# Optimization experiments

Measured on AMD Instinct MI355X. Metric: run time of the kernel, lower is better.

Reference implementation:

```python
import jax, jax.numpy as jnp
import numpy as np

H = 1024

def setup_inputs() -> dict:
    key = jax.random.key(0)
    ks = jax.random.split(key, 7)
    B, S = 64, 2048
    decoder_hidden = jax.random.normal(ks[0], (B, H), dtype=jnp.float32)
    encoder_outputs = jax.random.normal(ks[1], (B, S, H), dtype=jnp.float32)
    sc = 1.0 / np.sqrt(H)
    W1_w = jax.random.normal(ks[2], (H, H), dtype=jnp.float32) * sc
    W1_b = jax.random.normal(ks[3], (H,), dtype=jnp.float32) * sc
    W2_w = jax.random.normal(ks[4], (H, H), dtype=jnp.float32) * sc
    W2_b = jax.random.normal(ks[5], (H,), dtype=jnp.float32) * sc
    v_w = jax.random.normal(ks[6], (H,), dtype=jnp.float32) * sc
    return {"decoder_hidden": decoder_hidden, "encoder_outputs": encoder_outputs,
            "W1_w": W1_w, "W1_b": W1_b, "W2_w": W2_w, "W2_b": W2_b, "v_w": v_w}

def reference(decoder_hidden, encoder_outputs, W1_w, W1_b, W2_w, W2_b, v_w):
    # enc proj: [B,S,H] @ [H,H] ; dec proj: [B,H] @ [H,H], broadcast over S
    enc_proj = jnp.einsum('bsh,hk->bsk', encoder_outputs, W1_w) + W1_b
    dec_proj = decoder_hidden @ W2_w + W2_b  # [B,H]
    e = jnp.tanh(enc_proj + dec_proj[:, None, :])  # [B,S,H]
    scores = jnp.einsum('bsh,h->bs', e, v_w)  # [B,S]
    attn_weights = jax.nn.softmax(scores, axis=1)
    context = jnp.einsum('bs,bsh->bh', attn_weights, encoder_outputs)
    return (context, attn_weights)
```

## Files before the change

### kernel.cpp

```cpp
#include <hip/hip_runtime.h>
#include <hip/hip_bf16.h>
#include <hip/hip_fp16.h>

#define HDIM 1024
#define BATCH 64
#define SEQ 2048
#define MTOT (BATCH*SEQ)
#define BM 128
#define BN 256
#define BK 64
#define NKT (HDIM/BK)
#define NNT (HDIM/BN)

typedef float f32x4 __attribute__((ext_vector_type(4)));
typedef _Float16 half8 __attribute__((ext_vector_type(8)));
typedef _Float16 half4v __attribute__((ext_vector_type(4)));

static __device__ __forceinline__ void gload_lds16(const void* g, void* l) {
  __builtin_amdgcn_global_load_lds((const __attribute__((address_space(1))) void*)g,
                                   (__attribute__((address_space(3))) void*)l, 16, 0, 0);
}

__global__ void k_w1t(const float* __restrict__ W1, unsigned short* __restrict__ W1T) {
  __shared__ float tile[64][65];
  int h0 = blockIdx.x * 64, k0 = blockIdx.y * 64;
  int t = threadIdx.x;
#pragma unroll
  for (int j = 0; j < 4; ++j) {
    int q = j * 256 + t, r = q >> 4, c = (q & 15) * 4;
    float4 v = *(const float4*)(W1 + (size_t)(h0 + r) * HDIM + k0 + c);
    tile[r][c + 0] = v.x; tile[r][c + 1] = v.y; tile[r][c + 2] = v.z; tile[r][c + 3] = v.w;
  }
  __syncthreads();
#pragma unroll
  for (int j = 0; j < 4; ++j) {
    int q = j * 256 + t, r = q >> 4, c = (q & 15) * 4;
    union { _Float16 h[4]; ushort4 u; } cv;
    cv.h[0] = (_Float16)tile[c + 0][r];
    cv.h[1] = (_Float16)tile[c + 1][r];
    cv.h[2] = (_Float16)tile[c + 2][r];
    cv.h[3] = (_Float16)tile[c + 3][r];
    *(ushort4*)(W1T + (size_t)(k0 + r) * HDIM + h0 + c) = cv.u;
  }
}

__global__ void k_decproj(const float* __restrict__ dh, const float* __restrict__ W2,
                          const float* __restrict__ W2b, float* __restrict__ dp) {
  __shared__ float drow[HDIM];
  int b = blockIdx.x, t = threadIdx.x;
#pragma unroll
  for (int j = 0; j < 4; ++j) drow[j * 256 + t] = dh[(size_t)b * HDIM + j * 256 + t];
  __syncthreads();
  f32x4 acc = {0.f, 0.f, 0.f, 0.f};
#pragma unroll 16
  for (int h = 0; h < HDIM; ++h) {
    float d = drow[h];
    f32x4 w = *(const f32x4*)(W2 + (size_t)h * HDIM + t * 4);
    acc += w * d;
  }
  acc += *(const f32x4*)(W2b + t * 4);
  *(f32x4*)(dp + (size_t)b * HDIM + t * 4) = acc;
}

__global__ __launch_bounds__(512, 4) void k_scores(
    const float* __restrict__ E, const unsigned short* __restrict__ W1T,
    const float* __restrict__ W1b, const float* __restrict__ dp,
    const float* __restrict__ vw, float* __restrict__ spart,
    unsigned short* __restrict__ E16, int we16) {
  __shared__ __align__(16) _Float16 As[BM * BK];
  __shared__ __align__(16) unsigned short Bs[BN * BK];
  float (*scr)[4] = (float(*)[4])As;

  int t = threadIdx.x;
  int bid = blockIdx.x;
  int xcd = bid & 7;
  int q = bid >> 3;
  int mt = (xcd << 7) + (q >> 2);
  int nt = q & 3;
  int m0 = mt * BM, n0 = nt * BN;
  int b = m0 >> 11;

  int lane = t & 63, wid = t >> 6;
  int wr = wid >> 2, wc = wid & 3;
  int l15 = lane & 15, l4 = lane >> 4;

  f32x4 acc[4][4];
#pragma unroll
  for (int i = 0; i < 4; ++i)
#pragma unroll
    for (int j = 0; j < 4; ++j) acc[i][j] = {0.f, 0.f, 0.f, 0.f};

  int ar = t >> 4;
  int ac = (t & 15) * 4;
  int aswz = (((ac >> 3) ^ (ar & 7)) << 4) + ((ac & 7) << 1);
  const float* Ab = E + (size_t)m0 * HDIM;

  float4 areg[4];
#pragma unroll
  for (int j = 0; j < 4; ++j)
    areg[j] = *(const float4*)(Ab + (size_t)(j * 32 + ar) * HDIM + ac);

  for (int kt = 0; kt < NKT; ++kt) {
#pragma unroll
    for (int j = 0; j < 4; ++j) {
      int chunk = wid * 4 + j;
      int row = chunk * 8 + (lane >> 3);
      int u = (lane & 7) ^ (lane >> 3);
      const unsigned short* g = W1T + (size_t)(n0 + row) * HDIM + kt * BK + u * 8;
      gload_lds16(g, (char*)Bs + (size_t)chunk * 1024);
    }

#pragma unroll
    for (int j = 0; j < 4; ++j) {
      union { _Float16 h[4]; unsigned long long u64; } cv;
      cv.h[0] = (_Float16)areg[j].x; cv.h[1] = (_Float16)areg[j].y;
      cv.h[2] = (_Float16)areg[j].z; cv.h[3] = (_Float16)areg[j].w;
      *(unsigned long long*)((char*)As + (j * 32 + ar) * 128 + aswz) = cv.u64;
      if (we16 && j == nt)
        __builtin_nontemporal_store(cv.u64,
            (unsigned long long*)(E16 + (size_t)(m0 + j * 32 + ar) * HDIM + kt * BK + ac));
    }

    __syncthreads();

    int ktn = ((kt + 1) & (NKT - 1)) * BK;
#pragma unroll
    for (int j = 0; j < 4; ++j)
      areg[j] = *(const float4*)(Ab + (size_t)(j * 32 + ar) * HDIM + ktn + ac);

    __builtin_amdgcn_s_setprio(1);
#pragma unroll
    for (int ks = 0; ks < 2; ++ks) {
      half8 af[4], bf[4];
#pragma unroll
      for (int mi = 0; mi < 4; ++mi) {
        int row = wr * 64 + mi * 16 + l15;
        af[mi] = *(const half8*)((const char*)As + row * 128 + (((ks * 4 + l4) ^ (row & 7)) << 4));
      }
#pragma unroll
      for (int ni = 0; ni < 4; ++ni) {
        int row = wc * 64 + ni * 16 + l15;
        bf[ni] = *(const half8*)((const char*)Bs + row * 128 + (((ks * 4 + l4) ^ (row & 7)) << 4));
      }
#pragma unroll
      for (int mi = 0; mi < 4; ++mi)
#pragma unroll
        for (int ni = 0; ni < 4; ++ni)
          acc[mi][ni] = __builtin_amdgcn_mfma_f32_16x16x32_f16(af[mi], bf[ni], acc[mi][ni], 0, 0, 0);
    }
    __builtin_amdgcn_s_setprio(0);

    __syncthreads();
  }

  float bias_l[4], v_l[4];
#pragma unroll
  for (int ni = 0; ni < 4; ++ni) {
    int k = n0 + wc * 64 + ni * 16 + l15;
    bias_l[ni] = W1b[k] + dp[(size_t)b * HDIM + k];
    v_l[ni] = vw[k];
  }
#pragma unroll
  for (int mi = 0; mi < 4; ++mi) {
#pragma unroll
    for (int r = 0; r < 4; ++r) {
      float s = 0.f;
#pragma unroll
      for (int ni = 0; ni < 4; ++ni) {
        float x = acc[mi][ni][r] + bias_l[ni];
        float ex = __expf(2.f * x);
        float th = 1.f - 2.f / (ex + 1.f);
        s += th * v_l[ni];
      }
      s += __shfl_xor(s, 1); s += __shfl_xor(s, 2);
      s += __shfl_xor(s, 4); s += __shfl_xor(s, 8);
      if (l15 == 0) scr[wr * 64 + mi * 16 + l4 * 4 + r][wc] = s;
    }
  }
  __syncthreads();
  if (t < BM) {
    f32x4 p = *(const f32x4*)scr[t];
    spart[((size_t)m0 + t) * NNT + nt] = (p[0] + p[1]) + (p[2] + p[3]);
  }
}

__global__ void k_softmax(const float* __restrict__ spart, float* __restrict__ attn) {
  __shared__ float sc[SEQ];
  __shared__ float red[8];
  int b = blockIdx.x, t = threadIdx.x;
  float mx = -1e30f;
#pragma unroll
  for (int j = 0; j < 8; ++j) {
    int s = j * 256 + t;
    f32x4 x = *(const f32x4*)(spart + ((size_t)b * SEQ + s) * NNT);
    float v = (x[0] + x[1]) + (x[2] + x[3]);
    sc[s] = v;
    mx = fmaxf(mx, v);
  }
  for (int m = 1; m < 64; m <<= 1) mx = fmaxf(mx, __shfl_xor(mx, m));
  if ((t & 63) == 0) red[t >> 6] = mx;
  __syncthreads();
  mx = fmaxf(fmaxf(red[0], red[1]), fmaxf(red[2], red[3]));
  float w[8]; float sum = 0.f;
#pragma unroll
  for (int j = 0; j < 8; ++j) {
    float e = __expf(sc[j * 256 + t] - mx);
    w[j] = e; sum += e;
  }
  for (int m = 1; m < 64; m <<= 1) sum += __shfl_xor(sum, m);
  if ((t & 63) == 0) red[4 + (t >> 6)] = sum;
  __syncthreads();
  float inv = 1.f / (red[4] + red[5] + red[6] + red[7]);
#pragma unroll
  for (int j = 0; j < 8; ++j)
    attn[(size_t)b * SEQ + j * 256 + t] = w[j] * inv;
}

__global__ void k_ctx_part(const float* __restrict__ E, const float* __restrict__ attn,
                           float* __restrict__ cpart, int rpc) {
  int b = blockIdx.y, ch = blockIdx.x, nch = gridDim.x;
  int t = threadIdx.x;
  const float* wrow = attn + (size_t)b * SEQ + (size_t)ch * rpc;
  const float* Eb = E + ((size_t)b * SEQ + (size_t)ch * rpc) * HDIM;
  f32x4 acc = {0.f, 0.f, 0.f, 0.f};
#pragma unroll 4
  for (int s = 0; s < rpc; ++s) {
    float w = wrow[s];
    f32x4 e = *(const f32x4*)(Eb + (size_t)s * HDIM + t * 4);
    acc += e * w;
  }
  *(f32x4*)(cpart + ((size_t)b * nch + ch) * HDIM + t * 4) = acc;
}

__global__ void k_ctx_part16(const unsigned short* __restrict__ E16, const float* __restrict__ attn,
                             float* __restrict__ cpart, int rpc) {
  int b = blockIdx.y, ch = blockIdx.x, nch = gridDim.x;
  int t = threadIdx.x;
  const float* wrow = attn + (size_t)b * SEQ + (size_t)ch * rpc;
  const unsigned short* Eb = E16 + ((size_t)b * SEQ + (size_t)ch * rpc) * HDIM;
  f32x4 acc = {0.f, 0.f, 0.f, 0.f};
#pragma unroll 4
  for (int s = 0; s < rpc; ++s) {
    float w = wrow[s];
    half4v e = *(const half4v*)(Eb + (size_t)s * HDIM + t * 4);
    acc[0] += w * (float)e[0];
    acc[1] += w * (float)e[1];
    acc[2] += w * (float)e[2];
    acc[3] += w * (float)e[3];
  }
  *(f32x4*)(cpart + ((size_t)b * nch + ch) * HDIM + t * 4) = acc;
}

__global__ void k_ctx_reduce(const float* __restrict__ cpart, float* __restrict__ ctx, int nch) {
  int idx = blockIdx.x * 256 + threadIdx.x;
  int b = idx >> 10, k = idx & 1023;
  float s = 0.f;
  for (int c = 0; c < nch; ++c) s += cpart[((size_t)(b * nch + c)) * HDIM + k];
  ctx[idx] = s;
}

extern "C" void kernel_launch(void* const* d_in, const int* in_sizes, int n_in,
                              void* d_out, int out_size, void* d_ws, size_t ws_size,
                              hipStream_t stream) {
  const float* dh  = (const float*)d_in[0];
  const float* E   = (const float*)d_in[1];
  const float* W1w = (const float*)d_in[2];
  const float* W1b = (const float*)d_in[3];
  const float* W2w = (const float*)d_in[4];
  const float* W2b = (const float*)d_in[5];
  const float* vw  = (const float*)d_in[6];
  float* out  = (float*)d_out;
  float* ctx  = out;
  float* attn = out + BATCH * HDIM;

  char* ws = (char*)d_ws;
  unsigned short* W1T = (unsigned short*)ws;
  float* dp    = (float*)(ws + (2u << 20));
  float* spart = (float*)(ws + (2u << 20) + (256u << 10));
  float* cpart = (float*)(ws + (6u << 20) + (256u << 10));
  unsigned short* E16 = (unsigned short*)(ws + (14u << 20) + (256u << 10));

  size_t need32  = (6u << 20) + (256u << 10) + (size_t)BATCH * 32 * HDIM * 4;
  size_t needE16 = (14u << 20) + (256u << 10) + (size_t)MTOT * HDIM * 2;
  int nch = (ws_size >= need32) ? 32 : 16;
  int rpc = SEQ / nch;
  int use16 = (ws_size >= needE16) ? 1 : 0;

  k_w1t<<<dim3(16, 16), 256, 0, stream>>>(W1w, W1T);
  k_decproj<<<BATCH, 256, 0, stream>>>(dh, W2w, W2b, dp);
  k_scores<<<(MTOT / BM) * NNT, 512, 0, stream>>>(E, W1T, W1b, dp, vw, spart,
                                                  use16 ? E16 : W1T, use16);
  k_softmax<<<BATCH, 256, 0, stream>>>(spart, attn);
  if (use16)
    k_ctx_part16<<<dim3(nch, BATCH), 256, 0, stream>>>(E16, attn, cpart, rpc);
  else
    k_ctx_part<<<dim3(nch, BATCH), 256, 0, stream>>>(E, attn, cpart, rpc);
  k_ctx_reduce<<<256, 256, 0, stream>>>(cpart, ctx, nch);
}
```

Baseline: 517.4 us.

## Double-buffer LDS tiles and split GEMM k-loop into barrier-phased MFMA stages

Restructures the score GEMM main loop in `k_scores` to use double-buffered LDS for both the A (fp16 encoder) and B (W1T) tiles. The next tile's global loads and LDS conversions are issued while MFMAs run on the current buffer. Each k-step is split into four phases: fragment loads, then s_barrier, lgkmcnt wait and sched_barrier around a raised-priority MFMA group. This is meant to hide global and LDS latency behind matrix-core work, in the style of a wave ping-pong schedule. In exchange LDS use per block doubles and the occupancy hint drops from 4 to 2. Only `s_barrier` and lgkmcnt waits guard the async LDS loads, so correctness depends on the compiler inserting the needed vmcnt waits.

```diff
diff --git a/kernel.cpp b/kernel.cpp
--- a/kernel.cpp
+++ b/kernel.cpp
@@ -62,14 +62,14 @@
   *(f32x4*)(dp + (size_t)b * HDIM + t * 4) = acc;
 }
 
-__global__ __launch_bounds__(512, 4) void k_scores(
+__global__ __launch_bounds__(512, 2) void k_scores(
     const float* __restrict__ E, const unsigned short* __restrict__ W1T,
     const float* __restrict__ W1b, const float* __restrict__ dp,
     const float* __restrict__ vw, float* __restrict__ spart,
     unsigned short* __restrict__ E16, int we16) {
-  __shared__ __align__(16) _Float16 As[BM * BK];
-  __shared__ __align__(16) unsigned short Bs[BN * BK];
-  float (*scr)[4] = (float(*)[4])As;
+  __shared__ __align__(16) _Float16 Ab[2][BM * BK];
+  __shared__ __align__(16) unsigned short Bb[2][BN * BK];
+  float (*scr)[4] = (float(*)[4])Ab[0];
 
   int t = threadIdx.x;
   int bid = blockIdx.x;
@@ -93,64 +93,146 @@
   int ar = t >> 4;
   int ac = (t & 15) * 4;
   int aswz = (((ac >> 3) ^ (ar & 7)) << 4) + ((ac & 7) << 1);
-  const float* Ab = E + (size_t)m0 * HDIM;
+  const float* Abase = E + (size_t)m0 * HDIM;
+
+  int brow_in = lane >> 3;
+  int bu = (lane & 7) ^ brow_in;
 
   float4 areg[4];
 #pragma unroll
+  for (int j = 0; j < 4; ++j) {
+    int chunk = wid * 4 + j;
+    int row = chunk * 8 + brow_in;
+    gload_lds16(W1T + (size_t)(n0 + row) * HDIM + bu * 8, (char*)Bb[0] + (size_t)chunk * 1024);
+  }
+#pragma unroll
   for (int j = 0; j < 4; ++j)
-    areg[j] = *(const float4*)(Ab + (size_t)(j * 32 + ar) * HDIM + ac);
+    areg[j] = *(const float4*)(Abase + (size_t)(j * 32 + ar) * HDIM + ac);
+#pragma unroll
+  for (int j = 0; j < 4; ++j) {
+    union { _Float16 h[4]; unsigned long long u64; } cv;
+    cv.h[0] = (_Float16)areg[j].x; cv.h[1] = (_Float16)areg[j].y;
+    cv.h[2] = (_Float16)areg[j].z; cv.h[3] = (_Float16)areg[j].w;
+    *(unsigned long long*)((char*)Ab[0] + (j * 32 + ar) * 128 + aswz) = cv.u64;
+    if (we16 && j == nt)
+      __builtin_nontemporal_store(cv.u64,
+          (unsigned long long*)(E16 + (size_t)(m0 + j * 32 + ar) * HDIM + ac));
+  }
+  __syncthreads();
 
   for (int kt = 0; kt < NKT; ++kt) {
-#pragma unroll
-    for (int j = 0; j < 4; ++j) {
-      int chunk = wid * 4 + j;
-      int row = chunk * 8 + (lane >> 3);
-      int u = (lane & 7) ^ (lane >> 3);
-      const unsigned short* g = W1T + (size_t)(n0 + row) * HDIM + kt * BK + u * 8;
-      gload_lds16(g, (char*)Bs + (size_t)chunk * 1024);
-    }
-
-#pragma unroll
-    for (int j = 0; j < 4; ++j) {
-      union { _Float16 h[4]; unsigned long long u64; } cv;
-      cv.h[0] = (_Float16)areg[j].x; cv.h[1] = (_Float16)areg[j].y;
-      cv.h[2] = (_Float16)areg[j].z; cv.h[3] = (_Float16)areg[j].w;
-      *(unsigned long long*)((char*)As + (j * 32 + ar) * 128 + aswz) = cv.u64;
-      if (we16 && j == nt)
-        __builtin_nontemporal_store(cv.u64,
-            (unsigned long long*)(E16 + (size_t)(m0 + j * 32 + ar) * HDIM + kt * BK + ac));
-    }
-
-    __syncthreads();
-
-    int ktn = ((kt + 1) & (NKT - 1)) * BK;
-#pragma unroll
-    for (int j = 0; j < 4; ++j)
-      areg[j] = *(const float4*)(Ab + (size_t)(j * 32 + ar) * HDIM + ktn + ac);
-
+    const char* Ac = (const char*)Ab[kt & 1];
+    const char* Bc = (const char*)Bb[kt & 1];
+    char* Bd = (char*)Bb[(kt + 1) & 1];
+    char* Ad = (char*)Ab[(kt + 1) & 1];
+    bool pf = (kt + 1 < NKT);
+    int ktn = (kt + 1) * BK;
+    half8 af[4], bf0, bf1;
+
+#pragma unroll
+    for (int mi = 0; mi < 4; ++mi) {
+      int row = wr * 64 + mi * 16 + l15;
+      af[mi] = *(const half8*)(Ac + row * 128 + ((l4 ^ (row & 7)) << 4));
+    }
+    {
+      int r0 = wc * 64 + l15;
+      bf0 = *(const half8*)(Bc + r0 * 128 + ((l4 ^ (r0 & 7)) << 4));
+      int r1 = wc * 64 + 16 + l15;
+      bf1 = *(const half8*)(Bc + r1 * 128 + ((l4 ^ (r1 & 7)) << 4));
+    }
+    if (pf) {
+#pragma unroll
+      for (int j = 0; j < 4; ++j) {
+        int chunk = wid * 4 + j;
+        int row = chunk * 8 + brow_in;
+        gload_lds16(W1T + (size_t)(n0 + row) * HDIM + ktn + bu * 8, Bd + (size_t)chunk * 1024);
+      }
+#pragma unroll
+      for (int j = 0; j < 4; ++j)
+        areg[j] = *(const float4*)(Abase + (size_t)(j * 32 + ar) * HDIM + ktn + ac);
+    }
+    __builtin_amdgcn_s_barrier();
+    asm volatile("s_waitcnt lgkmcnt(0)" ::: "memory");
+    __builtin_amdgcn_sched_barrier(0);
     __builtin_amdgcn_s_setprio(1);
 #pragma unroll
-    for (int ks = 0; ks < 2; ++ks) {
-      half8 af[4], bf[4];
-#pragma unroll
-      for (int mi = 0; mi < 4; ++mi) {
-        int row = wr * 64 + mi * 16 + l15;
-        af[mi] = *(const half8*)((const char*)As + row * 128 + (((ks * 4 + l4) ^ (row & 7)) << 4));
+    for (int mi = 0; mi < 4; ++mi) {
+      acc[mi][0] = __builtin_amdgcn_mfma_f32_16x16x32_f16(af[mi], bf0, acc[mi][0], 0, 0, 0);
+      acc[mi][1] = __builtin_amdgcn_mfma_f32_16x16x32_f16(af[mi], bf1, acc[mi][1], 0, 0, 0);
+    }
+    __builtin_amdgcn_s_setprio(0);
+    __builtin_amdgcn_s_barrier();
+
+    {
+      int r0 = wc * 64 + 32 + l15;
+      bf0 = *(const half8*)(Bc + r0 * 128 + ((l4 ^ (r0 & 7)) << 4));
+      int r1 = wc * 64 + 48 + l15;
+      bf1 = *(const half8*)(Bc + r1 * 128 + ((l4 ^ (r1 & 7)) << 4));
+    }
+    __builtin_amdgcn_s_barrier();
+    asm volatile("s_waitcnt lgkmcnt(0)" ::: "memory");
+    __builtin_amdgcn_sched_barrier(0);
+    __builtin_amdgcn_s_setprio(1);
+#pragma unroll
+    for (int mi = 0; mi < 4; ++mi) {
+      acc[mi][2] = __builtin_amdgcn_mfma_f32_16x16x32_f16(af[mi], bf0, acc[mi][2], 0, 0, 0);
+      acc[mi][3] = __builtin_amdgcn_mfma_f32_16x16x32_f16(af[mi], bf1, acc[mi][3], 0, 0, 0);
+    }
+    __builtin_amdgcn_s_setprio(0);
+    __builtin_amdgcn_s_barrier();
+
+#pragma unroll
+    for (int mi = 0; mi < 4; ++mi) {
+      int row = wr * 64 + mi * 16 + l15;
+      af[mi] = *(const half8*)(Ac + row * 128 + (((4 + l4) ^ (row & 7)) << 4));
+    }
+    {
+      int r0 = wc * 64 + l15;
+      bf0 = *(const half8*)(Bc + r0 * 128 + (((4 + l4) ^ (r0 & 7)) << 4));
+      int r1 = wc * 64 + 16 + l15;
+      bf1 = *(const half8*)(Bc + r1 * 128 + (((4 + l4) ^ (r1 & 7)) << 4));
+    }
+    if (pf) {
+#pragma unroll
+      for (int j = 0; j < 4; ++j) {
+        union { _Float16 h[4]; unsigned long long u64; } cv;
+        cv.h[0] = (_Float16)areg[j].x; cv.h[1] = (_Float16)areg[j].y;
+        cv.h[2] = (_Float16)areg[j].z; cv.h[3] = (_Float16)areg[j].w;
+        *(unsigned long long*)(Ad + (j * 32 + ar) * 128 + aswz) = cv.u64;
+        if (we16 && j == nt)
+          __builtin_nontemporal_store(cv.u64,
+              (unsigned long long*)(E16 + (size_t)(m0 + j * 32 + ar) * HDIM + ktn + ac));
       }
-#pragma unroll
-      for (int ni = 0; ni < 4; ++ni) {
-        int row = wc * 64 + ni * 16 + l15;
-        bf[ni] = *(const half8*)((const char*)Bs + row * 128 + (((ks * 4 + l4) ^ (row & 7)) << 4));
-      }
-#pragma unroll
-      for (int mi = 0; mi < 4; ++mi)
-#pragma unroll
-        for (int ni = 0; ni < 4; ++ni)
-          acc[mi][ni] = __builtin_amdgcn_mfma_f32_16x16x32_f16(af[mi], bf[ni], acc[mi][ni], 0, 0, 0);
+    }
+    __builtin_amdgcn_s_barrier();
+    asm volatile("s_waitcnt lgkmcnt(0)" ::: "memory");
+    __builtin_amdgcn_sched_barrier(0);
+    __builtin_amdgcn_s_setprio(1);
+#pragma unroll
+    for (int mi = 0; mi < 4; ++mi) {
+      acc[mi][0] = __builtin_amdgcn_mfma_f32_16x16x32_f16(af[mi], bf0, acc[mi][0], 0, 0, 0);
+      acc[mi][1] = __builtin_amdgcn_mfma_f32_16x16x32_f16(af[mi], bf1, acc[mi][1], 0, 0, 0);
     }
     __builtin_amdgcn_s_setprio(0);
-
-    __syncthreads();
+    __builtin_amdgcn_s_barrier();
+
+    {
+      int r0 = wc * 64 + 32 + l15;
+      bf0 = *(const half8*)(Bc + r0 * 128 + (((4 + l4) ^ (r0 & 7)) << 4));
+      int r1 = wc * 64 + 48 + l15;
+      bf1 = *(const half8*)(Bc + r1 * 128 + (((4 + l4) ^ (r1 & 7)) << 4));
+    }
+    __builtin_amdgcn_s_barrier();
+    asm volatile("s_waitcnt lgkmcnt(0)" ::: "memory");
+    __builtin_amdgcn_sched_barrier(0);
+    __builtin_amdgcn_s_setprio(1);
+#pragma unroll
+    for (int mi = 0; mi < 4; ++mi) {
+      acc[mi][2] = __builtin_amdgcn_mfma_f32_16x16x32_f16(af[mi], bf0, acc[mi][2], 0, 0, 0);
+      acc[mi][3] = __builtin_amdgcn_mfma_f32_16x16x32_f16(af[mi], bf1, acc[mi][3], 0, 0, 0);
+    }
+    __builtin_amdgcn_s_setprio(0);
+    __builtin_amdgcn_s_barrier();
   }
 
   float bias_l[4], v_l[4];
```

New measurement: 792.4 us. +53.1%, slower.
